# Performance work log

Hardware: AMD Instinct MI355X
Metric: run time of the kernel (lower is better)

The kernel has to match this reference:

```python
import jax, jax.numpy as jnp
import numpy as np

B, INPLANES, H, W = 32, 1024, 14, 14
PLANES, WIDTH, OUTC = 256, 256, 1024   # width = planes*(base_width/64)*groups; OUTC = planes*4
BITS = (2, 4, 8)                        # bit_list -> lv = 2**bit per expert
GN_GROUPS = 4
EPS = 1e-5


def _qact(x, lv):
    # quantized ReLU (PACT-style, clip [0,1], lv uniform levels) with STE
    y = jnp.clip(x, 0.0, 1.0)
    q = jnp.round(y * (lv - 1)) / (lv - 1)
    return y + jax.lax.stop_gradient(q - y)


def _qw(w, lv):
    # symmetric per-tensor weight quantization with STE
    n = lv // 2 - 1
    if n < 1:
        n = 1
    s = jnp.max(jnp.abs(w)) + 1e-12
    q = jnp.round(w / s * n) / n * s
    return w + jax.lax.stop_gradient(q - w)


def _conv(x, w, stride=1, pad=0):
    return jax.lax.conv_general_dilated(
        x, w, (stride, stride), [(pad, pad), (pad, pad)],
        dimension_numbers=('NCHW', 'OIHW', 'NCHW'))


def _bn(x, g, b, m, v):
    # inference-mode BatchNorm2d with running stats
    inv = g / jnp.sqrt(v + EPS)
    return x * inv[:, None, None] + (b - m * inv)[:, None, None]


def _expert(x, lv, w1, w2, w3, bn1, bn2):
    # quantized Bottleneck expert: qrelu -> conv1x1 -> bn -> relu -> qrelu -> conv3x3 -> bn -> relu -> qrelu -> conv1x1
    h = _conv(_qact(x, lv), _qw(w1, lv))
    h = jax.nn.relu(_bn(h, *bn1))
    h = _conv(_qact(h, lv), _qw(w2, lv), stride=1, pad=1)
    h = jax.nn.relu(_bn(h, *bn2))
    return _conv(_qact(h, lv), _qw(w3, lv))


def setup_inputs() -> dict:
    key = jax.random.key(0)
    ks = jax.random.split(key, 16)
    return {
        'x': jax.random.normal(ks[0], (B, INPLANES, H, W), jnp.float32),
        'mask': jax.random.randint(ks[1], (B,), 0, len(BITS), jnp.int32),
        'w1': jax.random.normal(ks[2], (WIDTH, INPLANES, 1, 1), jnp.float32) * 0.03,
        'w2': jax.random.normal(ks[3], (WIDTH, WIDTH, 3, 3), jnp.float32) * 0.03,
        'w3': jax.random.normal(ks[4], (OUTC, WIDTH, 1, 1), jnp.float32) * 0.03,
        'bn1_g': jax.random.uniform(ks[5], (WIDTH,), jnp.float32, 0.5, 1.5),
        'bn1_b': jax.random.normal(ks[6], (WIDTH,), jnp.float32) * 0.1,
        'bn1_m': jax.random.normal(ks[7], (WIDTH,), jnp.float32) * 0.1,
        'bn1_v': jax.random.uniform(ks[8], (WIDTH,), jnp.float32, 0.5, 1.5),
        'bn2_g': jax.random.uniform(ks[9], (WIDTH,), jnp.float32, 0.5, 1.5),
        'bn2_b': jax.random.normal(ks[10], (WIDTH,), jnp.float32) * 0.1,
        'bn2_m': jax.random.normal(ks[11], (WIDTH,), jnp.float32) * 0.1,
        'bn2_v': jax.random.uniform(ks[12], (WIDTH,), jnp.float32, 0.5, 1.5),
        'gn_g': jax.random.uniform(ks[13], (OUTC,), jnp.float32, 0.5, 1.5),
        'gn_b': jax.random.normal(ks[14], (OUTC,), jnp.float32) * 0.1,
    }


def reference(x, mask, w1, w2, w3, bn1_g, bn1_b, bn1_m, bn1_v,
              bn2_g, bn2_b, bn2_m, bn2_v, gn_g, gn_b):
    bn1 = (bn1_g, bn1_b, bn1_m, bn1_v)
    bn2 = (bn2_g, bn2_b, bn2_m, bn2_v)
    # sparse MoE: per-sample mask selects one quantized expert; combine masked outputs
    out = jnp.zeros((x.shape[0], OUTC, x.shape[2], x.shape[3]), x.dtype)
    for e, bit in enumerate(BITS):
        sel = (mask == e).astype(x.dtype)[:, None, None, None]
        out = out + sel * _expert(x, 2 ** bit, w1, w2, w3, bn1, bn2)
    # GroupNorm(4, OUTC)
    b_, c_, h_, w_ = out.shape
    g = out.reshape(b_, GN_GROUPS, c_ // GN_GROUPS, h_, w_)
    mu = g.mean(axis=(2, 3, 4), keepdims=True)
    var = g.var(axis=(2, 3, 4), keepdims=True)
    g = (g - mu) / jnp.sqrt(var + EPS)
    out = g.reshape(b_, c_, h_, w_) * gn_g[:, None, None] + gn_b[:, None, None]
    # residual (downsample=None, inplanes == planes*expansion) + relu
    return jax.nn.relu(out + x)
```

## Files before the change

### kernel.cpp

```cpp
#include <hip/hip_runtime.h>
#include <hip/hip_bf16.h>

typedef __attribute__((ext_vector_type(8))) short short8;
typedef __attribute__((ext_vector_type(4))) float f32x4;

#define PIX  196
#define EPSN 1e-5f

#define BO_XQ   256
#define BO_H1Q  (BO_XQ + 12845056)
#define BO_H2Q  (BO_H1Q + 3211264)
#define BO_W1Q  (BO_H2Q + 3211264)
#define BO_GNS  (BO_W1Q + 1572864)
#define BO_PMAX (BO_GNS + 8192)
#define DO_W2Q  0
#define DO_W3Q  3538944

__device__ __forceinline__ float e_ascale(int e) { return e == 0 ? 3.f : (e == 1 ? 15.f : 255.f); }
__device__ __forceinline__ float e_nq(int e)     { return e == 0 ? 1.f : (e == 1 ? 7.f : 127.f); }

__device__ __forceinline__ f32x4 mfma16(short8 a, short8 b, f32x4 c) {
    return __builtin_amdgcn_mfma_f32_16x16x32_bf16(a, b, c, 0, 0, 0);
}
__device__ __forceinline__ float wmax_reduce(const char* wsb, int t) {
    const float* pm = (const float*)(wsb + BO_PMAX) + t * 48;
    float s = 0.f;
    #pragma unroll
    for (int k = 0; k < 48; ++k) s = fmaxf(s, pm[k]);
    return s + 1e-12f;
}
__device__ __forceinline__ float bf16s_to_f32(short h) {
    unsigned u = ((unsigned)(unsigned short)h) << 16;
    return __uint_as_float(u);
}

__global__ __launch_bounds__(1024) void maxabs_kernel(
        const float* __restrict__ w1, const float* __restrict__ w2,
        const float* __restrict__ w3, float* __restrict__ pmax) {
    int t = blockIdx.x / 48, j = blockIdx.x - t * 48;
    const float4* w4 = (const float4*)(t == 0 ? w1 : (t == 1 ? w2 : w3));
    int n4 = (t == 1) ? 147456 : 65536;
    float m = 0.f;
    for (int i = j * 1024 + threadIdx.x; i < n4; i += 48 * 1024) {
        float4 v = w4[i];
        m = fmaxf(m, fmaxf(fmaxf(fabsf(v.x), fabsf(v.y)), fmaxf(fabsf(v.z), fabsf(v.w))));
    }
    __shared__ float red[1024];
    red[threadIdx.x] = m;
    __syncthreads();
    for (int s = 512; s > 0; s >>= 1) {
        if (threadIdx.x < s) red[threadIdx.x] = fmaxf(red[threadIdx.x], red[threadIdx.x + s]);
        __syncthreads();
    }
    if (threadIdx.x == 0) pmax[t * 48 + j] = red[0];
}

__global__ __launch_bounds__(256) void prep_all(
        const float* __restrict__ w1, const float* __restrict__ w2,
        const float* __restrict__ w3, const float* __restrict__ x,
        const int* __restrict__ mask, char* wsb, char* doutb) {
    __shared__ float xs[64][197];
    int tid = threadIdx.x, bx = blockIdx.x;
    if (bx < 512) {
        int b = bx >> 4, c0 = (bx & 15) * 64;
        float ascale = e_ascale(mask[b]);
        for (int idx = tid; idx < 64 * 196; idx += 256) {
            int ci = idx / 196, p = idx - ci * 196;
            xs[ci][p] = x[((size_t)b * 1024 + c0 + ci) * 196 + p];
        }
        __syncthreads();
        __hip_bfloat16* xq = (__hip_bfloat16*)(wsb + BO_XQ);
        for (int idx = tid; idx < 196 * 64; idx += 256) {
            int p = idx / 64, ci = idx - p * 64;
            float v = fminf(fmaxf(xs[ci][p], 0.f), 1.f);
            xq[((size_t)b * 196 + p) * 1024 + c0 + ci] = __float2bfloat16(rintf(v * ascale));
        }
    } else if (bx < 1536) {
        int idx = (bx - 512) * 256 + tid;
        float s = wmax_reduce(wsb, 0);
        float v = w1[idx];
        __hip_bfloat16* dst = (__hip_bfloat16*)(wsb + BO_W1Q);
        #pragma unroll
        for (int e = 0; e < 3; ++e)
            dst[e * 262144 + idx] = __float2bfloat16(rintf(v / s * e_nq(e)));
    } else if (bx < 3840) {
        int idx = (bx - 1536) * 256 + tid;
        float s = wmax_reduce(wsb, 1);
        float v = w2[idx];
        int co = idx / 2304, r = idx - co * 2304, ci = r / 9, tap = r - ci * 9;
        __hip_bfloat16* dst = (__hip_bfloat16*)(doutb + DO_W2Q);
        size_t off = ((size_t)tap * 256 + co) * 256 + ci;
        #pragma unroll
        for (int e = 0; e < 3; ++e)
            dst[e * 589824 + off] = __float2bfloat16(rintf(v / s * e_nq(e)));
    } else {
        int idx = (bx - 3840) * 256 + tid;
        float s = wmax_reduce(wsb, 2);
        float v = w3[idx];
        __hip_bfloat16* dst = (__hip_bfloat16*)(doutb + DO_W3Q);
        #pragma unroll
        for (int e = 0; e < 3; ++e)
            dst[e * 262144 + idx] = __float2bfloat16(rintf(v / s * e_nq(e)));
    }
}

__global__ __launch_bounds__(256) void conv1_mfma(
        char* wsb, const int* __restrict__ mask,
        const float* __restrict__ bg, const float* __restrict__ bb,
        const float* __restrict__ bm, const float* __restrict__ bv) {
    int b = blockIdx.z;
    int e = mask[b];
    float ascale = e_ascale(e);
    float s1 = wmax_reduce(wsb, 0);
    float kscale = (s1 / e_nq(e)) / ascale;

    const short* xq  = (const short*)(wsb + BO_XQ) + (size_t)b * 196 * 1024;
    const short* w1q = (const short*)(wsb + BO_W1Q) + (size_t)e * 262144;
    __hip_bfloat16* h1q = (__hip_bfloat16*)(wsb + BO_H1Q) + (size_t)b * 196 * 256;

    __shared__ short As[64 * 136];
    __shared__ short Bs[64 * 136];

    int tid = threadIdx.x, w = tid >> 6, lane = tid & 63, r15 = lane & 15, g = lane >> 4;
    int mh = w >> 1, nh = w & 1;
    int px0 = blockIdx.x * 56, coB = blockIdx.y * 64;

    short8 ra[4], rb[4];
    auto load_tile = [&](int t) {
        int k0 = t * 128;
        #pragma unroll
        for (int ii = 0; ii < 4; ++ii) {
            int idx = ii * 256 + tid;
            int row = idx >> 4, c8 = (idx & 15) * 8;
            ra[ii] = *(const short8*)(xq + (size_t)min(px0 + row, 195) * 1024 + k0 + c8);
            rb[ii] = *(const short8*)(w1q + (size_t)(coB + row) * 1024 + k0 + c8);
        }
    };
    auto store_tile = [&]() {
        #pragma unroll
        for (int ii = 0; ii < 4; ++ii) {
            int idx = ii * 256 + tid;
            int row = idx >> 4, c8 = (idx & 15) * 8;
            *(short8*)(As + row * 136 + c8) = ra[ii];
            *(short8*)(Bs + row * 136 + c8) = rb[ii];
        }
    };

    f32x4 acc[2][2] = {};
    load_tile(0);
    for (int t = 0; t < 8; ++t) {
        __syncthreads();
        store_tile();
        __syncthreads();
        if (t < 7) load_tile(t + 1);
        #pragma unroll
        for (int ks = 0; ks < 4; ++ks) {
            short8 bf0 = *(const short8*)(Bs + (nh * 32 + r15) * 136 + ks * 32 + g * 8);
            short8 bf1 = *(const short8*)(Bs + (nh * 32 + 16 + r15) * 136 + ks * 32 + g * 8);
            #pragma unroll
            for (int m = 0; m < 2; ++m) {
                short8 af = *(const short8*)(As + (mh * 32 + m * 16 + r15) * 136 + ks * 32 + g * 8);
                acc[m][0] = mfma16(af, bf0, acc[m][0]);
                acc[m][1] = mfma16(af, bf1, acc[m][1]);
            }
        }
    }
    #pragma unroll
    for (int n = 0; n < 2; ++n) {
        int co = coB + nh * 32 + n * 16 + r15;
        float inv = bg[co] * rsqrtf(bv[co] + EPSN);
        float mm = kscale * inv;
        float beta = bb[co] - bm[co] * inv;
        #pragma unroll
        for (int m = 0; m < 2; ++m)
            #pragma unroll
            for (int r = 0; r < 4; ++r) {
                int s = mh * 32 + m * 16 + g * 4 + r, px = px0 + s;
                if (s < 56 && px < 196) {
                    float h = fmaxf(acc[m][n][r] * mm + beta, 0.f);
                    h1q[(size_t)px * 256 + co] = __float2bfloat16(rintf(fminf(h, 1.f) * ascale));
                }
            }
    }
}

__global__ __launch_bounds__(256) void conv2_mfma(
        char* wsb, const char* __restrict__ doutb, const int* __restrict__ mask,
        const float* __restrict__ bg, const float* __restrict__ bb,
        const float* __restrict__ bm, const float* __restrict__ bv) {
    int b = blockIdx.z;
    int e = mask[b];
    float ascale = e_ascale(e);
    float s2 = wmax_reduce(wsb, 1);
    float kscale = (s2 / e_nq(e)) / ascale;

    const short* h1q = (const short*)(wsb + BO_H1Q) + (size_t)b * 196 * 256;
    const short* w2q = (const short*)(doutb + DO_W2Q) + (size_t)e * 589824;
    __hip_bfloat16* h2q = (__hip_bfloat16*)(wsb + BO_H2Q) + (size_t)b * 196 * 256;

    __shared__ short Xs[6 * 16 * 40];
    __shared__ short Ws9[9 * 64 * 40];

    int tid = threadIdx.x, w = tid >> 6, lane = tid & 63, r15 = lane & 15, g = lane >> 4;
    int r0 = blockIdx.x * 4;
    int px0 = blockIdx.x * 56;
    int coB = blockIdx.y * 64;
    const short8 z8 = {0, 0, 0, 0, 0, 0, 0, 0};

    int wco = tid >> 2, wc8 = (tid & 3) * 8;

    int rr[4], cc[4];
    #pragma unroll
    for (int m = 0; m < 4; ++m) {
        int s0 = min(m * 16 + r15, 55);
        rr[m] = s0 / 14; cc[m] = s0 - rr[m] * 14;
    }

    short8 rx[2], rw[9];
    auto load_tile = [&](int sl) {
        int ci0 = sl * 32;
        #pragma unroll
        for (int ii = 0; ii < 2; ++ii) {
            int idx = ii * 256 + tid;
            rx[ii] = z8;
            if (idx < 384) {
                int xc = idx & 3, xsx = (idx >> 2) & 15, xsy = idx >> 6;
                int iy = r0 - 1 + xsy, ix = xsx - 1;
                if ((unsigned)iy < 14u && (unsigned)ix < 14u)
                    rx[ii] = *(const short8*)(h1q + (size_t)(iy * 14 + ix) * 256 + ci0 + xc * 8);
            }
        }
        #pragma unroll
        for (int tap = 0; tap < 9; ++tap)
            rw[tap] = *(const short8*)(w2q + ((size_t)tap * 256 + coB + wco) * 256 + ci0 + wc8);
    };
    auto store_tile = [&]() {
        #pragma unroll
        for (int ii = 0; ii < 2; ++ii) {
            int idx = ii * 256 + tid;
            if (idx < 384) {
                int xc = idx & 3, xsx = (idx >> 2) & 15, xsy = idx >> 6;
                *(short8*)(Xs + (xsy * 16 + xsx) * 40 + xc * 8) = rx[ii];
            }
        }
        #pragma unroll
        for (int tap = 0; tap < 9; ++tap)
            *(short8*)(Ws9 + (tap * 64 + wco) * 40 + wc8) = rw[tap];
    };

    f32x4 acc[4] = {};
    load_tile(0);
    for (int sl = 0; sl < 8; ++sl) {
        __syncthreads();
        store_tile();
        __syncthreads();
        if (sl < 7) load_tile(sl + 1);
        #pragma unroll
        for (int tap = 0; tap < 9; ++tap) {
            int ty = tap / 3, tx = tap - ty * 3;
            short8 bf = *(const short8*)(Ws9 + (tap * 64 + w * 16 + r15) * 40 + g * 8);
            #pragma unroll
            for (int m = 0; m < 4; ++m) {
                short8 af = *(const short8*)(Xs + ((rr[m] + ty) * 16 + cc[m] + tx) * 40 + g * 8);
                acc[m] = mfma16(af, bf, acc[m]);
            }
        }
    }
    int co = coB + w * 16 + r15;
    float inv = bg[co] * rsqrtf(bv[co] + EPSN);
    float mm = kscale * inv;
    float beta = bb[co] - bm[co] * inv;
    #pragma unroll
    for (int m = 0; m < 4; ++m)
        #pragma unroll
        for (int r = 0; r < 4; ++r) {
            int s = m * 16 + g * 4 + r, px = px0 + s;
            if (s < 56 && px < 196) {
                float h = fmaxf(acc[m][r] * mm + beta, 0.f);
                h2q[(size_t)px * 256 + co] = __float2bfloat16(rintf(fminf(h, 1.f) * ascale));
            }
        }
}

__global__ __launch_bounds__(256) void conv3_mfma(
        char* wsb, const char* __restrict__ doutb, const int* __restrict__ mask) {
    int b = blockIdx.z;
    int e = mask[b];
    float ascale = e_ascale(e);
    float s3 = wmax_reduce(wsb, 2);
    float kscale = (s3 / e_nq(e)) / ascale;

    const short* h2q = (const short*)(wsb + BO_H2Q) + (size_t)b * 196 * 256;
    const short* w3q = (const short*)(doutb + DO_W3Q) + (size_t)e * 262144;
    __hip_bfloat16* pg = (__hip_bfloat16*)(wsb + BO_XQ) + (size_t)b * 1024 * 196;

    __shared__ float Ct[128 * 58];
    __shared__ float rs[256], rss[256];
    short* As = (short*)Ct;
    short* Bs = As + 64 * 72;

    int tid = threadIdx.x, w = tid >> 6, lane = tid & 63, r15 = lane & 15, g = lane >> 4;
    int px0 = blockIdx.x * 56;
    int coQ = blockIdx.y * 128;
    int gslot = (b * 4 + (blockIdx.y >> 1)) * 8 + (blockIdx.y & 1) * 4 + blockIdx.x;

    short8 ra[2], rb[4];
    auto load_tile = [&](int t) {
        int k0 = t * 64;
        #pragma unroll
        for (int ii = 0; ii < 2; ++ii) {
            int idx = ii * 256 + tid;
            int arow = idx >> 3, ac = (idx & 7) * 8;
            ra[ii] = *(const short8*)(h2q + (size_t)min(px0 + arow, 195) * 256 + k0 + ac);
        }
        #pragma unroll
        for (int ii = 0; ii < 4; ++ii) {
            int idx = ii * 256 + tid;
            int brow = idx >> 3, bc = (idx & 7) * 8;
            rb[ii] = *(const short8*)(w3q + (size_t)(coQ + brow) * 256 + k0 + bc);
        }
    };
    auto store_tile = [&]() {
        #pragma unroll
        for (int ii = 0; ii < 2; ++ii) {
            int idx = ii * 256 + tid;
            *(short8*)(As + (idx >> 3) * 72 + (idx & 7) * 8) = ra[ii];
        }
        #pragma unroll
        for (int ii = 0; ii < 4; ++ii) {
            int idx = ii * 256 + tid;
            *(short8*)(Bs + (idx >> 3) * 72 + (idx & 7) * 8) = rb[ii];
        }
    };

    f32x4 acc[4][2] = {};
    load_tile(0);
    for (int t = 0; t < 4; ++t) {
        __syncthreads();
        store_tile();
        __syncthreads();
        if (t < 3) load_tile(t + 1);
        #pragma unroll
        for (int ks = 0; ks < 2; ++ks) {
            short8 bf0 = *(const short8*)(Bs + (w * 32 + r15) * 72 + ks * 32 + g * 8);
            short8 bf1 = *(const short8*)(Bs + (w * 32 + 16 + r15) * 72 + ks * 32 + g * 8);
            #pragma unroll
            for (int m = 0; m < 4; ++m) {
                short8 af = *(const short8*)(As + (m * 16 + r15) * 72 + ks * 32 + g * 8);
                acc[m][0] = mfma16(af, bf0, acc[m][0]);
                acc[m][1] = mfma16(af, bf1, acc[m][1]);
            }
        }
    }
    __syncthreads();
    #pragma unroll
    for (int n = 0; n < 2; ++n)
        #pragma unroll
        for (int m = 0; m < 4; ++m)
            #pragma unroll
            for (int r = 0; r < 4; ++r) {
                int s = m * 16 + g * 4 + r;
                if (s < 56) Ct[(w * 32 + n * 16 + r15) * 58 + s] = acc[m][n][r];
            }
    __syncthreads();
    float sum = 0.f, ss = 0.f;
    for (int idx = tid; idx < 128 * 56; idx += 256) {
        int col = idx / 56, s = idx - col * 56, px = px0 + s;
        if (px < 196) {
            float v = Ct[col * 58 + s] * kscale;
            __hip_bfloat16 hv = __float2bfloat16(v);
            float vq = __bfloat162float(hv);
            pg[(size_t)(coQ + col) * 196 + px] = hv;
            sum += vq; ss += vq * vq;
        }
    }
    rs[tid] = sum; rss[tid] = ss;
    __syncthreads();
    for (int st = 128; st > 0; st >>= 1) {
        if (tid < st) { rs[tid] += rs[tid + st]; rss[tid] += rss[tid + st]; }
        __syncthreads();
    }
    if (tid == 0) {
        float* gns = (float*)(wsb + BO_GNS);
        gns[gslot * 2] = rs[0];
        gns[gslot * 2 + 1] = rss[0];
    }
}

__global__ __launch_bounds__(256) void gn_apply(
        const char* __restrict__ wsb, const float* __restrict__ x,
        const float* __restrict__ gg, const float* __restrict__ gb,
        float* __restrict__ out) {
    int bgid = blockIdx.x >> 4, six = blockIdx.x & 15;
    int g = bgid & 3;
    const float* gns = (const float*)(wsb + BO_GNS);
    float S = 0.f, Q = 0.f;
    #pragma unroll
    for (int k = 0; k < 8; ++k) { S += gns[(bgid * 8 + k) * 2]; Q += gns[(bgid * 8 + k) * 2 + 1]; }
    float mu = S * (1.f / 50176.f);
    float var = Q * (1.f / 50176.f) - mu * mu;
    float rstd = rsqrtf(var + EPSN);

    const __hip_bfloat16* pg = (const __hip_bfloat16*)(wsb + BO_XQ) + (size_t)bgid * 50176;
    const float* xg = x + (size_t)bgid * 50176;
    float* og = out + (size_t)bgid * 50176;

    int tid = threadIdx.x;
    for (int i = tid; i < 392; i += 256) {
        int eb = six * 3136 + i * 8;
        int c = eb / 196, r = eb - c * 196;
        short8 hv = *(const short8*)(pg + eb);
        float4 x0 = *(const float4*)(xg + eb);
        float4 x1 = *(const float4*)(xg + eb + 4);
        float xv[8] = {x0.x, x0.y, x0.z, x0.w, x1.x, x1.y, x1.z, x1.w};
        float o[8];
        #pragma unroll
        for (int j = 0; j < 8; ++j) {
            int gc = g * 256 + c;
            float sc = gg[gc] * rstd;
            float sh = gb[gc] - mu * sc;
            float v = bf16s_to_f32(hv[j]);
            o[j] = fmaxf(v * sc + sh + xv[j], 0.f);
            if (++r == 196) { r = 0; ++c; }
        }
        *(float4*)(og + eb)     = make_float4(o[0], o[1], o[2], o[3]);
        *(float4*)(og + eb + 4) = make_float4(o[4], o[5], o[6], o[7]);
    }
}

extern "C" void kernel_launch(void* const* d_in, const int* in_sizes, int n_in,
                              void* d_out, int out_size, void* d_ws, size_t ws_size,
                              hipStream_t stream) {
    (void)in_sizes; (void)n_in; (void)out_size; (void)ws_size;
    const float* x    = (const float*)d_in[0];
    const int*   mask = (const int*)d_in[1];
    const float* w1   = (const float*)d_in[2];
    const float* w2   = (const float*)d_in[3];
    const float* w3   = (const float*)d_in[4];
    const float* b1g  = (const float*)d_in[5];
    const float* b1b  = (const float*)d_in[6];
    const float* b1m  = (const float*)d_in[7];
    const float* b1v  = (const float*)d_in[8];
    const float* b2g  = (const float*)d_in[9];
    const float* b2b  = (const float*)d_in[10];
    const float* b2m  = (const float*)d_in[11];
    const float* b2v  = (const float*)d_in[12];
    const float* gng  = (const float*)d_in[13];
    const float* gnb  = (const float*)d_in[14];
    char* wsb = (char*)d_ws;
    char* doutb = (char*)d_out;
    float* out = (float*)d_out;

    maxabs_kernel<<<144, 1024, 0, stream>>>(w1, w2, w3, (float*)(wsb + BO_PMAX));
    prep_all<<<4864, 256, 0, stream>>>(w1, w2, w3, x, mask, wsb, doutb);
    conv1_mfma<<<dim3(4, 4, 32), 256, 0, stream>>>(wsb, mask, b1g, b1b, b1m, b1v);
    conv2_mfma<<<dim3(4, 4, 32), 256, 0, stream>>>(wsb, doutb, mask, b2g, b2b, b2m, b2v);
    conv3_mfma<<<dim3(4, 8, 32), 256, 0, stream>>>(wsb, doutb, mask);
    gn_apply<<<2048, 256, 0, stream>>>(wsb, x, gng, gnb, out);
}
```

Before: 85.35 us.

## Halve conv2 output-channel tile, split waves 2x2, vectorize x loads in prep

```diff
diff --git a/kernel.cpp b/kernel.cpp
--- a/kernel.cpp
+++ b/kernel.cpp
@@ -64,9 +64,18 @@
     if (bx < 512) {
         int b = bx >> 4, c0 = (bx & 15) * 64;
         float ascale = e_ascale(mask[b]);
-        for (int idx = tid; idx < 64 * 196; idx += 256) {
+        const float4* xb4 = (const float4*)(x + ((size_t)b * 1024 + c0) * 196);
+        for (int i4 = tid; i4 < 3136; i4 += 256) {
+            float4 v = xb4[i4];
+            int idx = i4 * 4;
             int ci = idx / 196, p = idx - ci * 196;
-            xs[ci][p] = x[((size_t)b * 1024 + c0 + ci) * 196 + p];
+            xs[ci][p] = v.x;
+            int p1 = p + 1, c1 = ci; if (p1 == 196) { p1 = 0; ++c1; }
+            xs[c1][p1] = v.y;
+            int p2 = p1 + 1, c2 = c1; if (p2 == 196) { p2 = 0; ++c2; }
+            xs[c2][p2] = v.z;
+            int p3 = p2 + 1, c3 = c2; if (p3 == 196) { p3 = 0; ++c3; }
+            xs[c3][p3] = v.w;
         }
         __syncthreads();
         __hip_bfloat16* xq = (__hip_bfloat16*)(wsb + BO_XQ);
@@ -198,25 +207,24 @@
     const short* w2q = (const short*)(doutb + DO_W2Q) + (size_t)e * 589824;
     __hip_bfloat16* h2q = (__hip_bfloat16*)(wsb + BO_H2Q) + (size_t)b * 196 * 256;
 
-    __shared__ short Xs[6 * 16 * 40];
-    __shared__ short Ws9[9 * 64 * 40];
+    __shared__ short Xs[6 * 16 * 34];
+    __shared__ short Ws9[9 * 32 * 34];
 
     int tid = threadIdx.x, w = tid >> 6, lane = tid & 63, r15 = lane & 15, g = lane >> 4;
+    int mh = w >> 1, nh = w & 1;
     int r0 = blockIdx.x * 4;
     int px0 = blockIdx.x * 56;
-    int coB = blockIdx.y * 64;
+    int coB = blockIdx.y * 32;
     const short8 z8 = {0, 0, 0, 0, 0, 0, 0, 0};
 
-    int wco = tid >> 2, wc8 = (tid & 3) * 8;
-
-    int rr[4], cc[4];
-    #pragma unroll
-    for (int m = 0; m < 4; ++m) {
-        int s0 = min(m * 16 + r15, 55);
+    int rr[2], cc[2];
+    #pragma unroll
+    for (int m = 0; m < 2; ++m) {
+        int s0 = min(mh * 32 + m * 16 + r15, 55);
         rr[m] = s0 / 14; cc[m] = s0 - rr[m] * 14;
     }
 
-    short8 rx[2], rw[9];
+    short8 rx[2], rw[5];
     auto load_tile = [&](int sl) {
         int ci0 = sl * 32;
         #pragma unroll
@@ -231,8 +239,13 @@
             }
         }
         #pragma unroll
-        for (int tap = 0; tap < 9; ++tap)
-            rw[tap] = *(const short8*)(w2q + ((size_t)tap * 256 + coB + wco) * 256 + ci0 + wc8);
+        for (int ii = 0; ii < 5; ++ii) {
+            int idx = ii * 256 + tid;
+            if (idx < 1152) {
+                int tap = idx >> 7, rem = idx & 127, co = rem >> 2, c8 = (rem & 3) * 8;
+                rw[ii] = *(const short8*)(w2q + ((size_t)tap * 256 + coB + co) * 256 + ci0 + c8);
+            }
+        }
     };
     auto store_tile = [&]() {
         #pragma unroll
@@ -240,15 +253,20 @@
             int idx = ii * 256 + tid;
             if (idx < 384) {
                 int xc = idx & 3, xsx = (idx >> 2) & 15, xsy = idx >> 6;
-                *(short8*)(Xs + (xsy * 16 + xsx) * 40 + xc * 8) = rx[ii];
-            }
-        }
-        #pragma unroll
-        for (int tap = 0; tap < 9; ++tap)
-            *(short8*)(Ws9 + (tap * 64 + wco) * 40 + wc8) = rw[tap];
-    };
-
-    f32x4 acc[4] = {};
+                *(short8*)(Xs + (xsy * 16 + xsx) * 34 + xc * 8) = rx[ii];
+            }
+        }
+        #pragma unroll
+        for (int ii = 0; ii < 5; ++ii) {
+            int idx = ii * 256 + tid;
+            if (idx < 1152) {
+                int tap = idx >> 7, rem = idx & 127, co = rem >> 2, c8 = (rem & 3) * 8;
+                *(short8*)(Ws9 + (tap * 32 + co) * 34 + c8) = rw[ii];
+            }
+        }
+    };
+
+    f32x4 acc[2] = {};
     load_tile(0);
     for (int sl = 0; sl < 8; ++sl) {
         __syncthreads();
@@ -258,23 +276,23 @@
         #pragma unroll
         for (int tap = 0; tap < 9; ++tap) {
             int ty = tap / 3, tx = tap - ty * 3;
-            short8 bf = *(const short8*)(Ws9 + (tap * 64 + w * 16 + r15) * 40 + g * 8);
+            short8 bf = *(const short8*)(Ws9 + (tap * 32 + nh * 16 + r15) * 34 + g * 8);
             #pragma unroll
-            for (int m = 0; m < 4; ++m) {
-                short8 af = *(const short8*)(Xs + ((rr[m] + ty) * 16 + cc[m] + tx) * 40 + g * 8);
+            for (int m = 0; m < 2; ++m) {
+                short8 af = *(const short8*)(Xs + ((rr[m] + ty) * 16 + cc[m] + tx) * 34 + g * 8);
                 acc[m] = mfma16(af, bf, acc[m]);
             }
         }
     }
-    int co = coB + w * 16 + r15;
+    int co = coB + nh * 16 + r15;
     float inv = bg[co] * rsqrtf(bv[co] + EPSN);
     float mm = kscale * inv;
     float beta = bb[co] - bm[co] * inv;
     #pragma unroll
-    for (int m = 0; m < 4; ++m)
+    for (int m = 0; m < 2; ++m)
         #pragma unroll
         for (int r = 0; r < 4; ++r) {
-            int s = m * 16 + g * 4 + r, px = px0 + s;
+            int s = mh * 32 + m * 16 + g * 4 + r, px = px0 + s;
             if (s < 56 && px < 196) {
                 float h = fmaxf(acc[m][r] * mm + beta, 0.f);
                 h2q[(size_t)px * 256 + co] = __float2bfloat16(rintf(fminf(h, 1.f) * ascale));
@@ -454,7 +472,7 @@
     maxabs_kernel<<<144, 1024, 0, stream>>>(w1, w2, w3, (float*)(wsb + BO_PMAX));
     prep_all<<<4864, 256, 0, stream>>>(w1, w2, w3, x, mask, wsb, doutb);
     conv1_mfma<<<dim3(4, 4, 32), 256, 0, stream>>>(wsb, mask, b1g, b1b, b1m, b1v);
-    conv2_mfma<<<dim3(4, 4, 32), 256, 0, stream>>>(wsb, doutb, mask, b2g, b2b, b2m, b2v);
+    conv2_mfma<<<dim3(4, 8, 32), 256, 0, stream>>>(wsb, doutb, mask, b2g, b2b, b2m, b2v);
     conv3_mfma<<<dim3(4, 8, 32), 256, 0, stream>>>(wsb, doutb, mask);
     gn_apply<<<2048, 256, 0, stream>>>(wsb, x, gng, gnb, out);
 }
```

Measured after the change: 96.25 us. 12.8% more time.
